# Optimization experiments

Measured on AMD Instinct MI355X. Metric: run time of the kernel, lower is better.

## Reference

```python
import jax, jax.numpy as jnp
import numpy as np

N_NODES = 8192
N_EDGES = 262144
N_ADJ = 2
BATCH = 16
D_IN = 32
D_OUT = 64
D_EMB = 64


def setup_inputs() -> dict:
    key = jax.random.key(0)
    ks = jax.random.split(key, 6)
    edge_row = jax.random.randint(ks[0], (N_ADJ, N_EDGES), 0, N_NODES, dtype=jnp.int32)
    edge_col = jax.random.randint(ks[1], (N_ADJ, N_EDGES), 0, N_NODES, dtype=jnp.int32)
    edge_w = jax.random.uniform(ks[2], (N_ADJ, N_EDGES), dtype=jnp.float32)
    X = jax.random.normal(ks[3], (BATCH, D_IN, N_NODES), dtype=jnp.float32)
    Z = jax.random.normal(ks[4], (N_NODES, D_EMB), dtype=jnp.float32)
    stdv = 1.0 / np.sqrt(D_OUT)
    W = jax.random.uniform(ks[5], (D_IN, D_OUT), dtype=jnp.float32, minval=-stdv, maxval=stdv)
    return {"edge_row": edge_row, "edge_col": edge_col, "edge_w": edge_w,
            "X": X, "Z": Z, "W": W}


def reference(edge_row, edge_col, edge_w, X, Z, W):
    batch, d, n = X.shape
    X0 = X.reshape(-1, n)  # [b*d, n]

    def spmm(row, col, w, V):
        # sparse A @ V with A in COO form; V: [n, m] -> [n, m]
        return jax.ops.segment_sum(w[:, None] * V[col], row, num_segments=n)

    terms = [X0]
    for k in range(edge_row.shape[0]):  # small fixed loop over supports
        X1 = spmm(edge_row[k], edge_col[k], edge_w[k], X0.T).T  # [b*d, n]
        X2 = 2.0 * spmm(edge_row[k], edge_col[k], edge_w[k], X1.T).T - X0
        terms += [X1, X2]

    # adaptive adjacency: column-normalized softmax of relu(Z Z^T)
    Az = jax.nn.softmax(jax.nn.relu(Z @ Z.T), axis=0)  # [n, n]
    Xz = (Az @ X0.T).T  # [b*d, n]
    terms.append(Xz)

    Xcat = jnp.stack(terms, axis=2)  # [b*d, n, 2*nA+2]
    Xs = Xcat.sum(2).reshape(batch, d, n).transpose(0, 2, 1)  # [batch, n, d]
    return Xs @ W  # [batch, n, out_features]
```

## Files before the change

kernel.cpp:

```cpp
#include <hip/hip_runtime.h>

#define NN 8192
#define NE 262144
#define BD 512
#define DE 64

typedef __attribute__((ext_vector_type(8))) short short8;
typedef __attribute__((ext_vector_type(4))) short short4v;
typedef __attribute__((ext_vector_type(16))) float float16;

#define MFMA(a, b, c) __builtin_amdgcn_mfma_f32_32x32x16_bf16(a, b, c, 0, 0, 0)

static __device__ __forceinline__ unsigned short f2b(float x) {
  unsigned u = __float_as_uint(x);
  return (unsigned short)((u + 0x7fffu + ((u >> 16) & 1u)) >> 16);
}
static __device__ __forceinline__ float b2f(unsigned short h) {
  return __uint_as_float(((unsigned)h) << 16);
}

__global__ void k_transpose(const float* __restrict__ X, float* __restrict__ Y0,
                            float* __restrict__ Ysum) {
  __shared__ float t[32][33];
  int n0 = blockIdx.x * 32, f0 = blockIdx.y * 32;
  int tx = threadIdx.x, ty = threadIdx.y;
#pragma unroll
  for (int yy = 0; yy < 4; yy++)
    t[ty + 8 * yy][tx] = X[(size_t)(f0 + ty + 8 * yy) * NN + n0 + tx];
  __syncthreads();
#pragma unroll
  for (int yy = 0; yy < 4; yy++) {
    float v = t[tx][ty + 8 * yy];
    size_t o = (size_t)(n0 + ty + 8 * yy) * BD + f0 + tx;
    Y0[o] = v;
    Ysum[o] = -v;
  }
}

__global__ void k_cast(const float* __restrict__ X, unsigned short* __restrict__ Y0bT) {
  size_t t = (size_t)(blockIdx.x * 256 + threadIdx.x) * 8;
  float4 a = *(const float4*)(X + t);
  float4 b = *(const float4*)(X + t + 4);
  short8 v;
  v[0] = (short)f2b(a.x); v[1] = (short)f2b(a.y);
  v[2] = (short)f2b(a.z); v[3] = (short)f2b(a.w);
  v[4] = (short)f2b(b.x); v[5] = (short)f2b(b.y);
  v[6] = (short)f2b(b.z); v[7] = (short)f2b(b.w);
  *(short8*)(Y0bT + t) = v;
}

__global__ void k_zsplit(const float* __restrict__ Z, unsigned short* __restrict__ Zh,
                         unsigned short* __restrict__ Zl) {
  size_t t = (size_t)(blockIdx.x * 256 + threadIdx.x) * 4;
  float4 a = *(const float4*)(Z + t);
  float f[4] = {a.x, a.y, a.z, a.w};
  short4v hv, lv;
#pragma unroll
  for (int i = 0; i < 4; i++) {
    unsigned short hh = f2b(f[i]);
    hv[i] = (short)hh;
    lv[i] = (short)f2b(f[i] - b2f(hh));
  }
  *(short4v*)(Zh + t) = hv;
  *(short4v*)(Zl + t) = lv;
}

__global__ __launch_bounds__(256) void k_colsum(const unsigned short* __restrict__ Zh,
                                                const unsigned short* __restrict__ Zl,
                                                float* __restrict__ ssum) {
  int jt = blockIdx.x;
  int chunk = blockIdx.y;
  int tid = threadIdx.x;
  int w = tid >> 6, lane = tid & 63, li = lane & 31, h = lane >> 5;
  int jb = jt * 64 + (w & 1) * 32 + li;
  short8 bjh[4], bjl[4];
#pragma unroll
  for (int ks = 0; ks < 4; ks++) {
    bjh[ks] = *(const short8*)(Zh + (size_t)jb * DE + ks * 16 + 8 * h);
    bjl[ks] = *(const short8*)(Zl + (size_t)jb * DE + ks * 16 + 8 * h);
  }
  float csum = 0.f;
  for (int it = 0; it < 32; it++) {
    int ib = chunk * 2048 + (w >> 1) * 32 + it * 64 + li;
    short8 aih[4], ail[4];
#pragma unroll
    for (int ks = 0; ks < 4; ks++) {
      aih[ks] = *(const short8*)(Zh + (size_t)ib * DE + ks * 16 + 8 * h);
      ail[ks] = *(const short8*)(Zl + (size_t)ib * DE + ks * 16 + 8 * h);
    }
    float16 s;
#pragma unroll
    for (int r = 0; r < 16; r++) s[r] = 0.f;
#pragma unroll
    for (int ks = 0; ks < 4; ks++) {
      s = MFMA(aih[ks], bjh[ks], s);
      s = MFMA(aih[ks], bjl[ks], s);
      s = MFMA(ail[ks], bjh[ks], s);
    }
#pragma unroll
    for (int r = 0; r < 16; r++)
      csum += __expf(fminf(fmaxf(s[r], 0.f), 80.f));
  }
  csum += __shfl_xor(csum, 32);
  if (lane < 32) atomicAdd(ssum + jb, csum);
}

__global__ void k_inv(const float* __restrict__ ssum, float* __restrict__ invs) {
  int i = blockIdx.x * 256 + threadIdx.x;
  invs[i] = 1.0f / ssum[i];
}

__global__ void k_hist(const int* __restrict__ erow, int* __restrict__ cnt) {
  int t = blockIdx.x * 256 + threadIdx.x;
  int k = t >> 18;
  atomicAdd(cnt + k * NN + erow[t], 1);
}

#define RPS 8208
__global__ __launch_bounds__(256) void k_scan(const int* __restrict__ cnt,
                                              int* __restrict__ rowptr,
                                              int* __restrict__ fill) {
  int k = blockIdx.x;
  const int* c = cnt + k * NN;
  int* rp = rowptr + k * RPS;
  int* fl = fill + k * NN;
  __shared__ int part[256];
  int t = threadIdx.x;
  int local[32];
  int s = 0;
#pragma unroll
  for (int i = 0; i < 32; i++) { local[i] = c[t * 32 + i]; s += local[i]; }
  part[t] = s;
  __syncthreads();
  for (int off = 1; off < 256; off <<= 1) {
    int v = (t >= off) ? part[t - off] : 0;
    __syncthreads();
    part[t] += v;
    __syncthreads();
  }
  int run = (t == 0) ? 0 : part[t - 1];
#pragma unroll
  for (int i = 0; i < 32; i++) {
    rp[t * 32 + i] = run;
    fl[t * 32 + i] = run;
    run += local[i];
  }
  if (t == 255) rp[NN] = run;
}

__global__ void k_scatter(const int* __restrict__ erow, const int* __restrict__ ecol,
                          const float* __restrict__ ew, int* __restrict__ fill,
                          int* __restrict__ ecol_s, float* __restrict__ ew_s) {
  int t = blockIdx.x * 256 + threadIdx.x;
  int k = t >> 18;
  int r = erow[t];
  int pos = atomicAdd(fill + k * NN + r, 1);
  ecol_s[(size_t)k * NE + pos] = ecol[t];
  ew_s[(size_t)k * NE + pos] = ew[t];
}

__global__ __launch_bounds__(256) void k_csr(const int* __restrict__ rowptr,
                                             const int* __restrict__ cols,
                                             const float* __restrict__ w,
                                             const float* __restrict__ src,
                                             float* __restrict__ dst,
                                             const float* __restrict__ extra,
                                             float scale) {
  int wid = threadIdx.x >> 6;
  int lane = threadIdx.x & 63;
  int row = blockIdx.x * 4 + wid;
  int start = rowptr[row], end = rowptr[row + 1];
  float a0x = 0.f, a0y = 0.f, a0z = 0.f, a0w = 0.f;
  float a1x = 0.f, a1y = 0.f, a1z = 0.f, a1w = 0.f;
  for (int e = start; e < end; e++) {
    int c = __builtin_amdgcn_readfirstlane(cols[e]);
    float wv = w[e];
    const float4* s = (const float4*)(src + (size_t)c * BD);
    float4 v0 = s[lane], v1 = s[lane + 64];
    a0x += wv * v0.x; a0y += wv * v0.y; a0z += wv * v0.z; a0w += wv * v0.w;
    a1x += wv * v1.x; a1y += wv * v1.y; a1z += wv * v1.z; a1w += wv * v1.w;
  }
  float4* d = (float4*)(dst + (size_t)row * BD);
  if (extra) {
    const float4* ex = (const float4*)(extra + (size_t)row * BD);
    float4 e0 = ex[lane], e1 = ex[lane + 64];
    float4 d0 = d[lane], d1 = d[lane + 64];
    d0.x += scale * a0x + e0.x; d0.y += scale * a0y + e0.y;
    d0.z += scale * a0z + e0.z; d0.w += scale * a0w + e0.w;
    d1.x += scale * a1x + e1.x; d1.y += scale * a1y + e1.y;
    d1.z += scale * a1z + e1.z; d1.w += scale * a1w + e1.w;
    d[lane] = d0; d[lane + 64] = d1;
  } else {
    float4 d0 = {a0x, a0y, a0z, a0w};
    float4 d1 = {a1x, a1y, a1z, a1w};
    d[lane] = d0; d[lane + 64] = d1;
  }
}

__global__ __launch_bounds__(256) void k2(const unsigned short* __restrict__ Zh,
                                          const unsigned short* __restrict__ Zl,
                                          const unsigned short* __restrict__ Y0bT,
                                          const float* __restrict__ invs,
                                          float* __restrict__ Ysum) {
  __shared__ unsigned short P[32 * 128];
  int i0 = blockIdx.x * 32;
  int f0 = blockIdx.y * 256;
  int tid = threadIdx.x;
  int w = tid >> 6, lane = tid & 63, li = lane & 31, h = lane >> 5;

  short8 aih[4], ail[4];
#pragma unroll
  for (int ks = 0; ks < 4; ks++) {
    aih[ks] = *(const short8*)(Zh + (size_t)(i0 + li) * DE + ks * 16 + 8 * h);
    ail[ks] = *(const short8*)(Zl + (size_t)(i0 + li) * DE + ks * 16 + 8 * h);
  }
  float16 acc0, acc1;
#pragma unroll
  for (int r = 0; r < 16; r++) { acc0[r] = 0.f; acc1[r] = 0.f; }

  for (int js = 0; js < 64; js++) {
    int j0 = js * 128;
    int jj = j0 + w * 32 + li;
    short8 bjh[4], bjl[4];
#pragma unroll
    for (int ks = 0; ks < 4; ks++) {
      bjh[ks] = *(const short8*)(Zh + (size_t)jj * DE + ks * 16 + 8 * h);
      bjl[ks] = *(const short8*)(Zl + (size_t)jj * DE + ks * 16 + 8 * h);
    }
    float16 s;
#pragma unroll
    for (int r = 0; r < 16; r++) s[r] = 0.f;
#pragma unroll
    for (int ks = 0; ks < 4; ks++) {
      s = MFMA(aih[ks], bjh[ks], s);
      s = MFMA(aih[ks], bjl[ks], s);
      s = MFMA(ail[ks], bjh[ks], s);
    }
    float iv = invs[jj];
#pragma unroll
    for (int r = 0; r < 16; r++) {
      float pv = __expf(fminf(fmaxf(s[r], 0.f), 80.f)) * iv;
      int il = (r & 3) + 8 * (r >> 2) + 4 * h;
      P[(il * 128 + w * 32 + li) ^ ((il & 7) * 8)] = f2b(pv);
    }
    __syncthreads();
#pragma unroll
    for (int ks2 = 0; ks2 < 8; ks2++) {
      short8 af = *(const short8*)(P + ((li * 128 + ks2 * 16 + 8 * h) ^ ((li & 7) * 8)));
      const unsigned short* bp =
          Y0bT + (size_t)(f0 + w * 64 + li) * NN + j0 + ks2 * 16 + 8 * h;
      short8 bf0 = *(const short8*)bp;
      short8 bf1 = *(const short8*)(bp + (size_t)32 * NN);
      acc0 = MFMA(af, bf0, acc0);
      acc1 = MFMA(af, bf1, acc1);
    }
    __syncthreads();
  }
#pragma unroll
  for (int r = 0; r < 16; r++) {
    int i = i0 + (r & 3) + 8 * (r >> 2) + 4 * h;
    int f = f0 + w * 64 + li;
    Ysum[(size_t)i * BD + f] += acc0[r];
    Ysum[(size_t)i * BD + f + 32] += acc1[r];
  }
}

__global__ void k3(const float* __restrict__ Ysum, const float* __restrict__ W,
                   float* __restrict__ out) {
  __shared__ float yt[32][68];
  __shared__ float wt[32][68];
  int n0 = blockIdx.x * 64;
  int b = blockIdx.y;
  int tid = threadIdx.x;
#pragma unroll
  for (int q = 0; q < 2; q++) {
    int flat = (q * 256 + tid) * 4;
    int r = flat >> 5, c = flat & 31;
    float4 a = *(const float4*)(Ysum + (size_t)(n0 + r) * BD + b * 32 + c);
    yt[c + 0][r] = a.x; yt[c + 1][r] = a.y; yt[c + 2][r] = a.z; yt[c + 3][r] = a.w;
    int rd = flat >> 6, co = flat & 63;
    *(float4*)&wt[rd][co] = *(const float4*)(W + rd * 64 + co);
  }
  __syncthreads();
  int tx = tid & 15, ty = tid >> 4;
  float acc[4][4];
#pragma unroll
  for (int a = 0; a < 4; a++)
#pragma unroll
    for (int bq = 0; bq < 4; bq++) acc[a][bq] = 0.f;
#pragma unroll
  for (int d = 0; d < 32; d++) {
    float4 a = *(const float4*)&yt[d][ty * 4];
    float4 w4 = *(const float4*)&wt[d][tx * 4];
    float av[4] = {a.x, a.y, a.z, a.w}, wv[4] = {w4.x, w4.y, w4.z, w4.w};
#pragma unroll
    for (int nn = 0; nn < 4; nn++)
#pragma unroll
      for (int oo = 0; oo < 4; oo++) acc[nn][oo] += av[nn] * wv[oo];
  }
#pragma unroll
  for (int nn = 0; nn < 4; nn++) {
    float4 v = {acc[nn][0], acc[nn][1], acc[nn][2], acc[nn][3]};
    *(float4*)(out + (size_t)b * NN * 64 + (size_t)(n0 + ty * 4 + nn) * 64 + tx * 4) = v;
  }
}

extern "C" void kernel_launch(void* const* d_in, const int* in_sizes, int n_in,
                              void* d_out, int out_size, void* d_ws, size_t ws_size,
                              hipStream_t stream) {
  const int* erow = (const int*)d_in[0];
  const int* ecol = (const int*)d_in[1];
  const float* ew = (const float*)d_in[2];
  const float* X = (const float*)d_in[3];
  const float* Z = (const float*)d_in[4];
  const float* W = (const float*)d_in[5];
  float* out = (float*)d_out;

  char* p = (char*)d_ws;
  float* Y0 = (float*)p;            p += (size_t)NN * BD * 4;
  float* Ysum = (float*)p;          p += (size_t)NN * BD * 4;
  float* Y1 = (float*)p;            p += (size_t)NN * BD * 4;
  unsigned short* Y0bT = (unsigned short*)p; p += (size_t)BD * NN * 2;
  unsigned short* Zh = (unsigned short*)p;   p += (size_t)NN * DE * 2;
  unsigned short* Zl = (unsigned short*)p;   p += (size_t)NN * DE * 2;
  float* ssum = (float*)p;          p += NN * 4;
  float* invs = (float*)p;          p += NN * 4;
  int* cnt = (int*)p;               p += 2 * NN * 4;
  int* rowptr = (int*)p;            p += 2 * RPS * 4;
  int* fill = (int*)p;              p += 2 * NN * 4;
  int* ecol_s = (int*)p;            p += (size_t)2 * NE * 4;
  float* ew_s = (float*)p;          p += (size_t)2 * NE * 4;

  k_transpose<<<dim3(NN / 32, BD / 32), dim3(32, 8), 0, stream>>>(X, Y0, Ysum);
  k_cast<<<(NN * BD / 8) / 256, 256, 0, stream>>>(X, Y0bT);
  k_zsplit<<<(NN * DE / 4) / 256, 256, 0, stream>>>(Z, Zh, Zl);
  hipMemsetAsync(ssum, 0, NN * sizeof(float), stream);
  hipMemsetAsync(cnt, 0, 2 * NN * sizeof(int), stream);
  k_hist<<<2 * NE / 256, 256, 0, stream>>>(erow, cnt);
  k_scan<<<2, 256, 0, stream>>>(cnt, rowptr, fill);
  k_scatter<<<2 * NE / 256, 256, 0, stream>>>(erow, ecol, ew, fill, ecol_s, ew_s);
  k_colsum<<<dim3(128, 4), 256, 0, stream>>>(Zh, Zl, ssum);
  k_inv<<<NN / 256, 256, 0, stream>>>(ssum, invs);
  for (int k = 0; k < 2; k++) {
    const int* rp = rowptr + k * RPS;
    const int* cs = ecol_s + (size_t)k * NE;
    const float* ws = ew_s + (size_t)k * NE;
    k_csr<<<NN / 4, 256, 0, stream>>>(rp, cs, ws, Y0, Y1, nullptr, 1.0f);
    k_csr<<<NN / 4, 256, 0, stream>>>(rp, cs, ws, Y1, Ysum, Y1, 2.0f);
  }
  k2<<<dim3(NN / 32, 2), 256, 0, stream>>>(Zh, Zl, Y0bT, invs, Ysum);
  k3<<<dim3(NN / 64, 16), 256, 0, stream>>>(Ysum, W, out);
}
```

Measured before the change: 845.7 us.

## Restructure dense attention kernel to keep P in registers with permlane swaps

The adaptive-adjacency kernel is reorganised so each wave computes the score tile transposed (j rows, i columns), converts it to bf16 in registers with packed converts, and rearranges it through permlane32 swaps into an MFMA A operand. This removes the shared-memory staging of P and the two block barriers per j-step. Each wave now accumulates all 256 output features for its own j-slice, and a cross-wave shared-memory reduction runs once at the end. It also changes the launch to a 1D grid with i-tile/f-half interleaving and moves the bf16 cast of X just before k2. The price is eight float16 accumulators per wave, so register pressure is high, and the launch bound asks for two blocks per SIMD.

```diff
diff --git a/kernel.cpp b/kernel.cpp
--- a/kernel.cpp
+++ b/kernel.cpp
@@ -197,71 +197,95 @@
   }
 }
 
-__global__ __launch_bounds__(256) void k2(const unsigned short* __restrict__ Zh,
-                                          const unsigned short* __restrict__ Zl,
-                                          const unsigned short* __restrict__ Y0bT,
-                                          const float* __restrict__ invs,
-                                          float* __restrict__ Ysum) {
-  __shared__ unsigned short P[32 * 128];
-  int i0 = blockIdx.x * 32;
-  int f0 = blockIdx.y * 256;
+__global__ __launch_bounds__(256, 2) void k2(const unsigned short* __restrict__ Zh,
+                                             const unsigned short* __restrict__ Zl,
+                                             const unsigned short* __restrict__ Y0bT,
+                                             const float* __restrict__ invs,
+                                             float* __restrict__ Ysum) {
+  __shared__ float red[4][32][33];
+  int bid = blockIdx.x;
+  int fhalf = bid & 1;
+  int itile = bid >> 1;
+  int i0 = itile * 32;
+  int f0 = fhalf * 256;
   int tid = threadIdx.x;
   int w = tid >> 6, lane = tid & 63, li = lane & 31, h = lane >> 5;
 
-  short8 aih[4], ail[4];
+  short8 bih[4], bil[4];
 #pragma unroll
   for (int ks = 0; ks < 4; ks++) {
-    aih[ks] = *(const short8*)(Zh + (size_t)(i0 + li) * DE + ks * 16 + 8 * h);
-    ail[ks] = *(const short8*)(Zl + (size_t)(i0 + li) * DE + ks * 16 + 8 * h);
-  }
-  float16 acc0, acc1;
-#pragma unroll
-  for (int r = 0; r < 16; r++) { acc0[r] = 0.f; acc1[r] = 0.f; }
-
-  for (int js = 0; js < 64; js++) {
-    int j0 = js * 128;
-    int jj = j0 + w * 32 + li;
-    short8 bjh[4], bjl[4];
+    bih[ks] = *(const short8*)(Zh + (size_t)(i0 + li) * DE + ks * 16 + 8 * h);
+    bil[ks] = *(const short8*)(Zl + (size_t)(i0 + li) * DE + ks * 16 + 8 * h);
+  }
+  float16 acc[8];
+#pragma unroll
+  for (int ft = 0; ft < 8; ft++)
+#pragma unroll
+    for (int r = 0; r < 16; r++) acc[ft][r] = 0.f;
+
+#pragma unroll 1
+  for (int t = 0; t < 64; t++) {
+    int jb = t * 128 + w * 32;
+    short8 ajh[4], ajl[4];
 #pragma unroll
     for (int ks = 0; ks < 4; ks++) {
-      bjh[ks] = *(const short8*)(Zh + (size_t)jj * DE + ks * 16 + 8 * h);
-      bjl[ks] = *(const short8*)(Zl + (size_t)jj * DE + ks * 16 + 8 * h);
+      ajh[ks] = *(const short8*)(Zh + (size_t)(jb + li) * DE + ks * 16 + 8 * h);
+      ajl[ks] = *(const short8*)(Zl + (size_t)(jb + li) * DE + ks * 16 + 8 * h);
     }
     float16 s;
 #pragma unroll
     for (int r = 0; r < 16; r++) s[r] = 0.f;
 #pragma unroll
     for (int ks = 0; ks < 4; ks++) {
-      s = MFMA(aih[ks], bjh[ks], s);
-      s = MFMA(aih[ks], bjl[ks], s);
-      s = MFMA(ail[ks], bjh[ks], s);
-    }
-    float iv = invs[jj];
+      s = MFMA(ajh[ks], bih[ks], s);
+      s = MFMA(ajh[ks], bil[ks], s);
+      s = MFMA(ajl[ks], bih[ks], s);
+    }
+    unsigned wds[8];
+#pragma unroll
+    for (int q = 0; q < 8; q++) {
+      int r0 = q * 2;
+      int jl0 = 2 * (q & 1) + 8 * (q >> 1) + 4 * h;
+      float iv0 = invs[jb + jl0];
+      float iv1 = invs[jb + jl0 + 1];
+      float p0 = __expf(fminf(fmaxf(s[r0], 0.f), 80.f)) * iv0;
+      float p1 = __expf(fminf(fmaxf(s[r0 + 1], 0.f), 80.f)) * iv1;
+      asm("v_cvt_pk_bf16_f32 %0, %1, %2" : "=v"(wds[q]) : "v"(p0), "v"(p1));
+    }
+#pragma unroll
+    for (int ks2 = 0; ks2 < 2; ks2++) {
+      unsigned A0 = wds[ks2 * 4 + 0], A1 = wds[ks2 * 4 + 1];
+      unsigned A2 = wds[ks2 * 4 + 2], A3 = wds[ks2 * 4 + 3];
+      asm("v_permlane32_swap_b32 %0, %1" : "+v"(A0), "+v"(A2));
+      asm("v_permlane32_swap_b32 %0, %1" : "+v"(A1), "+v"(A3));
+      union { unsigned u[4]; short8 s8; } fu;
+      fu.u[0] = A0; fu.u[1] = A1; fu.u[2] = A2; fu.u[3] = A3;
+#pragma unroll
+      for (int ft = 0; ft < 8; ft++) {
+        const unsigned short* bp =
+            Y0bT + (size_t)(f0 + ft * 32 + li) * NN + jb + ks2 * 16 + 8 * h;
+        short8 B = *(const short8*)bp;
+        acc[ft] = MFMA(fu.s8, B, acc[ft]);
+      }
+    }
+  }
+#pragma unroll 1
+  for (int ft = 0; ft < 8; ft++) {
+    __syncthreads();
 #pragma unroll
     for (int r = 0; r < 16; r++) {
-      float pv = __expf(fminf(fmaxf(s[r], 0.f), 80.f)) * iv;
-      int il = (r & 3) + 8 * (r >> 2) + 4 * h;
-      P[(il * 128 + w * 32 + li) ^ ((il & 7) * 8)] = f2b(pv);
+      int ir = (r & 3) + 8 * (r >> 2) + 4 * h;
+      red[w][ir][li] = acc[ft][r];
     }
     __syncthreads();
 #pragma unroll
-    for (int ks2 = 0; ks2 < 8; ks2++) {
-      short8 af = *(const short8*)(P + ((li * 128 + ks2 * 16 + 8 * h) ^ ((li & 7) * 8)));
-      const unsigned short* bp =
-          Y0bT + (size_t)(f0 + w * 64 + li) * NN + j0 + ks2 * 16 + 8 * h;
-      short8 bf0 = *(const short8*)bp;
-      short8 bf1 = *(const short8*)(bp + (size_t)32 * NN);
-      acc0 = MFMA(af, bf0, acc0);
-      acc1 = MFMA(af, bf1, acc1);
-    }
-    __syncthreads();
-  }
-#pragma unroll
-  for (int r = 0; r < 16; r++) {
-    int i = i0 + (r & 3) + 8 * (r >> 2) + 4 * h;
-    int f = f0 + w * 64 + li;
-    Ysum[(size_t)i * BD + f] += acc0[r];
-    Ysum[(size_t)i * BD + f + 32] += acc1[r];
+    for (int q = 0; q < 4; q++) {
+      int e = q * 256 + tid;
+      int row = e >> 5, col = e & 31;
+      float sv = red[0][row][col] + red[1][row][col] +
+                 red[2][row][col] + red[3][row][col];
+      Ysum[(size_t)(i0 + row) * BD + f0 + ft * 32 + col] += sv;
+    }
   }
 }
 
@@ -317,22 +341,21 @@
   float* out = (float*)d_out;
 
   char* p = (char*)d_ws;
-  float* Y0 = (float*)p;            p += (size_t)NN * BD * 4;
-  float* Ysum = (float*)p;          p += (size_t)NN * BD * 4;
-  float* Y1 = (float*)p;            p += (size_t)NN * BD * 4;
+  float* Y0 = (float*)p;                     p += (size_t)NN * BD * 4;
+  float* Ysum = (float*)p;                   p += (size_t)NN * BD * 4;
+  float* Y1 = (float*)p;                     p += (size_t)NN * BD * 4;
   unsigned short* Y0bT = (unsigned short*)p; p += (size_t)BD * NN * 2;
   unsigned short* Zh = (unsigned short*)p;   p += (size_t)NN * DE * 2;
   unsigned short* Zl = (unsigned short*)p;   p += (size_t)NN * DE * 2;
-  float* ssum = (float*)p;          p += NN * 4;
-  float* invs = (float*)p;          p += NN * 4;
-  int* cnt = (int*)p;               p += 2 * NN * 4;
-  int* rowptr = (int*)p;            p += 2 * RPS * 4;
-  int* fill = (int*)p;              p += 2 * NN * 4;
-  int* ecol_s = (int*)p;            p += (size_t)2 * NE * 4;
-  float* ew_s = (float*)p;          p += (size_t)2 * NE * 4;
+  float* ssum = (float*)p;                   p += NN * 4;
+  float* invs = (float*)p;                   p += NN * 4;
+  int* cnt = (int*)p;                        p += 2 * NN * 4;
+  int* rowptr = (int*)p;                     p += 2 * RPS * 4;
+  int* fill = (int*)p;                       p += 2 * NN * 4;
+  int* ecol_s = (int*)p;                     p += (size_t)2 * NE * 4;
+  float* ew_s = (float*)p;                   p += (size_t)2 * NE * 4;
 
   k_transpose<<<dim3(NN / 32, BD / 32), dim3(32, 8), 0, stream>>>(X, Y0, Ysum);
-  k_cast<<<(NN * BD / 8) / 256, 256, 0, stream>>>(X, Y0bT);
   k_zsplit<<<(NN * DE / 4) / 256, 256, 0, stream>>>(Z, Zh, Zl);
   hipMemsetAsync(ssum, 0, NN * sizeof(float), stream);
   hipMemsetAsync(cnt, 0, 2 * NN * sizeof(int), stream);
@@ -348,6 +371,7 @@
     k_csr<<<NN / 4, 256, 0, stream>>>(rp, cs, ws, Y0, Y1, nullptr, 1.0f);
     k_csr<<<NN / 4, 256, 0, stream>>>(rp, cs, ws, Y1, Ysum, Y1, 2.0f);
   }
-  k2<<<dim3(NN / 32, 2), 256, 0, stream>>>(Zh, Zl, Y0bT, invs, Ysum);
+  k_cast<<<(NN * BD / 8) / 256, 256, 0, stream>>>(X, Y0bT);
+  k2<<<512, 256, 0, stream>>>(Zh, Zl, Y0bT, invs, Ysum);
   k3<<<dim3(NN / 64, 16), 256, 0, stream>>>(Ysum, W, out);
 }
```

New measurement: 913.2 us. 1.08x slower.
